# Kernel optimization log

Hardware: AMD Instinct MI355X
Metric: run time of the kernel (lower is better)

## Reference

```python
import jax, jax.numpy as jnp
import numpy as np

N, E, F_IN = 50000, 800000, 128
H, C, CLS, G = 8, 32, 16, 64
NEG_SLOPE = 0.2


def setup_inputs() -> dict:
    key = jax.random.key(0)
    ks = jax.random.split(key, 11)
    s = 0.05
    return {
        "x": jax.random.normal(ks[0], (N, F_IN), jnp.float32),
        "edge_index": jax.random.randint(ks[1], (2, E), 0, N, jnp.int32),
        "batch": jnp.sort(jax.random.randint(ks[2], (N,), 0, G, jnp.int32)),
        "W1": jax.random.normal(ks[3], (F_IN, H * C), jnp.float32) * s,
        "a1_src": jax.random.normal(ks[4], (H, C), jnp.float32) * s,
        "a1_dst": jax.random.normal(ks[5], (H, C), jnp.float32) * s,
        "b1": jax.random.normal(ks[6], (H * C,), jnp.float32) * s,
        "W2": jax.random.normal(ks[7], (H * C, CLS), jnp.float32) * s,
        "a2_src": jax.random.normal(ks[8], (1, CLS), jnp.float32) * s,
        "a2_dst": jax.random.normal(ks[9], (1, CLS), jnp.float32) * s,
        "b2": jax.random.normal(ks[10], (CLS,), jnp.float32) * s,
    }


def _gat_conv(x, src, dst, W, a_s, a_d, b, concat):
    n = x.shape[0]
    Hh, Cc = a_s.shape
    xp = (x @ W).reshape(n, Hh, Cc)                      # [N,H,C]
    al_s = jnp.einsum("nhc,hc->nh", xp, a_s)             # [N,H]
    al_d = jnp.einsum("nhc,hc->nh", xp, a_d)
    e = jax.nn.leaky_relu(al_s[src] + al_d[dst], NEG_SLOPE)  # [E,H]
    m = jax.ops.segment_max(e, dst, num_segments=n)      # segment softmax over dst
    ex = jnp.exp(e - m[dst])
    denom = jax.ops.segment_sum(ex, dst, num_segments=n)
    alpha = ex / denom[dst]                              # [E,H]
    out = jax.ops.segment_sum(xp[src] * alpha[:, :, None], dst, num_segments=n)
    out = out.reshape(n, Hh * Cc) if concat else out.mean(axis=1)
    return out + b


def reference(x, edge_index, batch, W1, a1_src, a1_dst, b1, W2, a2_src, a2_dst, b2):
    n = x.shape[0]
    loops = jnp.arange(n, dtype=edge_index.dtype)        # PyG add_self_loops=True
    ei = jnp.concatenate([edge_index, jnp.stack([loops, loops])], axis=1)
    src, dst = ei[0], ei[1]
    h = jax.nn.elu(_gat_conv(x, src, dst, W1, a1_src, a1_dst, b1, True))
    h = _gat_conv(h, src, dst, W2, a2_src, a2_dst, b2, False)
    counts = jax.ops.segment_sum(jnp.ones((n,), h.dtype), batch, num_segments=G)
    pooled = jax.ops.segment_sum(h, batch, num_segments=G) / jnp.maximum(counts, 1.0)[:, None]
    return jax.nn.log_softmax(pooled, axis=1)
```

## Files before the change

kernel.cpp:

```cpp
#include <hip/hip_runtime.h>
#include <math.h>

#define N_NODES 50000
#define N_EDGES 800000
#define FDIM 128
#define NH 8
#define NC 32
#define D1 256
#define NCLS 16
#define NGRP 64
#define NEG 0.2f
#define E_TOT (N_EDGES + N_NODES)
#define NB_N 196
#define G1_BLOCKS 782
#define E_CHUNK 4096
#define NCHUNK 196
#define NBIN 196

typedef __attribute__((ext_vector_type(8))) unsigned short u16x8;
typedef __attribute__((ext_vector_type(4))) unsigned short u16x4;
typedef __attribute__((ext_vector_type(8))) short short8;
typedef __attribute__((ext_vector_type(4))) float f32x4;

static __device__ __forceinline__ float bf2f(unsigned short u) {
    return __uint_as_float(((unsigned int)u) << 16);
}
static __device__ __forceinline__ unsigned short f2bf(float f) {
    unsigned int b = __float_as_uint(f);
    return (unsigned short)((b + 0x7FFFu + ((b >> 16) & 1u)) >> 16);
}

__global__ __launch_bounds__(256) void k_init(
    const float* __restrict__ W1, unsigned short* __restrict__ w1p,
    float* __restrict__ poolS, float* __restrict__ poolC,
    const int* __restrict__ ei, int* __restrict__ binmat) {
    __shared__ int h[NBIN];
    int c = blockIdx.x;
    for (int b = threadIdx.x; b < NBIN; b += 256) h[b] = 0;
    __syncthreads();
    int e0 = c * E_CHUNK;
    int e1 = e0 + E_CHUNK; if (e1 > N_EDGES) e1 = N_EDGES;
    for (int e = e0 + threadIdx.x; e < e1; e += 256)
        atomicAdd(&h[ei[N_EDGES + e] >> 8], 1);
    int i = blockIdx.x * 256 + threadIdx.x;
    if (i < NGRP * NCLS) poolS[i] = 0.f;
    if (i < NGRP) poolC[i] = 0.f;
    if (i < FDIM * D1) {
        int ks = i >> 13;
        int r = i & 8191;
        int nt2 = r >> 9;
        int r2 = r & 511;
        int lane = r2 >> 3, e = r2 & 7;
        int k = ks * 32 + (lane >> 4) * 8 + e;
        int col = nt2 * 16 + (lane & 15);
        w1p[i] = f2bf(W1[k * D1 + col]);
    }
    __syncthreads();
    for (int b = threadIdx.x; b < NBIN; b += 256) binmat[b * NCHUNK + c] = h[b];
}

__global__ __launch_bounds__(256) void k_binprescan(int* __restrict__ binmat,
                                                    int* __restrict__ binTot) {
    __shared__ int sh[256];
    int b = blockIdx.x, t = threadIdx.x;
    int v = (t < NCHUNK) ? binmat[b * NCHUNK + t] : 0;
    sh[t] = v;
    __syncthreads();
    for (int d = 1; d < 256; d <<= 1) {
        int tv = (t >= d) ? sh[t - d] : 0;
        __syncthreads();
        sh[t] += tv;
        __syncthreads();
    }
    if (t < NCHUNK) binmat[b * NCHUNK + t] = sh[t] - v;
    if (t == 255) binTot[b] = sh[255];
}

__global__ __launch_bounds__(256) void k_gemm1m(
    const float* __restrict__ x, const unsigned short* __restrict__ w1p,
    const float* __restrict__ a1s, const float* __restrict__ a1d,
    unsigned short* __restrict__ xp1b, float* __restrict__ al1s,
    float* __restrict__ al1d) {
    const int l = threadIdx.x & 63;
    const int wid = threadIdx.x >> 6;
    const int wr = wid >> 1, wc = wid & 1;
    const int l15 = l & 15, l4 = l >> 4;
    const int base = blockIdx.x * 64;
    const int r0 = base + wr * 32;

    f32x4 acc[2][8] = {};
#pragma unroll
    for (int ks = 0; ks < 4; ++ks) {
        const int kk = ks * 32 + l4 * 8;
        short8 af[2];
#pragma unroll
        for (int rt = 0; rt < 2; ++rt) {
            int row = r0 + rt * 16 + l15;
            float4 v0 = make_float4(0.f, 0.f, 0.f, 0.f), v1 = v0;
            if (row < N_NODES) {
                const float* xr = x + (size_t)row * FDIM + kk;
                v0 = *(const float4*)xr;
                v1 = *(const float4*)(xr + 4);
            }
            short8 a;
            a[0] = (short)f2bf(v0.x); a[1] = (short)f2bf(v0.y);
            a[2] = (short)f2bf(v0.z); a[3] = (short)f2bf(v0.w);
            a[4] = (short)f2bf(v1.x); a[5] = (short)f2bf(v1.y);
            a[6] = (short)f2bf(v1.z); a[7] = (short)f2bf(v1.w);
            af[rt] = a;
        }
#pragma unroll
        for (int nt = 0; nt < 8; ++nt) {
            int nt2 = wc * 8 + nt;
            short8 bf_ = *(const short8*)&w1p[(size_t)((ks * 16 + nt2) * 64 + l) * 8];
            acc[0][nt] = __builtin_amdgcn_mfma_f32_16x16x32_bf16(af[0], bf_, acc[0][nt], 0, 0, 0);
            acc[1][nt] = __builtin_amdgcn_mfma_f32_16x16x32_bf16(af[1], bf_, acc[1][nt], 0, 0, 0);
        }
    }
#pragma unroll
    for (int rt = 0; rt < 2; ++rt) {
        int rbase = r0 + rt * 16 + l4 * 4;
#pragma unroll
        for (int nt = 0; nt < 8; ++nt) {
            int col = wc * 128 + nt * 16 + l15;
            f32x4 c = acc[rt][nt];
#pragma unroll
            for (int r = 0; r < 4; ++r) {
                int row = rbase + r;
                if (row < N_NODES) xp1b[(size_t)row * D1 + col] = f2bf(c[r]);
            }
        }
    }
#pragma unroll
    for (int hl = 0; hl < 4; ++hl) {
        int hg = wc * 4 + hl;
        float as0 = a1s[hg * NC + l15], as1 = a1s[hg * NC + 16 + l15];
        float ad0 = a1d[hg * NC + l15], ad1 = a1d[hg * NC + 16 + l15];
#pragma unroll
        for (int rt = 0; rt < 2; ++rt) {
            f32x4 c0 = acc[rt][2 * hl], c1 = acc[rt][2 * hl + 1];
#pragma unroll
            for (int r = 0; r < 4; ++r) {
                float ss = c0[r] * as0 + c1[r] * as1;
                float dd = c0[r] * ad0 + c1[r] * ad1;
#pragma unroll
                for (int msk = 1; msk < 16; msk <<= 1) {
                    ss += __shfl_xor(ss, msk);
                    dd += __shfl_xor(dd, msk);
                }
                int row = r0 + rt * 16 + l4 * 4 + r;
                if (l15 == 0 && row < N_NODES) {
                    al1s[row * NH + hg] = ss;
                    al1d[row * NH + hg] = dd;
                }
            }
        }
    }
}

__global__ __launch_bounds__(256) void k_binscatter(const int* __restrict__ ei,
                                                    const int* __restrict__ offs,
                                                    const int* __restrict__ binTot,
                                                    int* __restrict__ binned) {
    __shared__ int cur[NBIN];
    __shared__ int sb[256];
    int c = blockIdx.x;
    int t = threadIdx.x;
    int v = (t < NBIN) ? binTot[t] : 0;
    sb[t] = v;
    __syncthreads();
    for (int d = 1; d < 256; d <<= 1) {
        int tv = (t >= d) ? sb[t - d] : 0;
        __syncthreads();
        sb[t] += tv;
        __syncthreads();
    }
    if (t < NBIN) cur[t] = (sb[t] - v) + offs[t * NCHUNK + c];
    __syncthreads();
    int e0 = c * E_CHUNK;
    int e1 = e0 + E_CHUNK; if (e1 > N_EDGES) e1 = N_EDGES;
    for (int e = e0 + t; e < e1; e += 256) {
        int s = ei[e], d = ei[N_EDGES + e];
        int pos = atomicAdd(&cur[d >> 8], 1);
        binned[pos] = s | ((d & 255) << 16);
    }
}

__global__ __launch_bounds__(256) void k_bincsr(const int* __restrict__ binTot,
                                                const int* __restrict__ binned,
                                                int* __restrict__ rowptr,
                                                int* __restrict__ cnt,
                                                int* __restrict__ esrc) {
    __shared__ int sh[256];
    __shared__ int lcnt[256];
    __shared__ int lcur[256];
    int b = blockIdx.x;
    int t = threadIdx.x;
    int v = (t < NBIN) ? binTot[t] : 0;
    sh[t] = v;
    __syncthreads();
    for (int d = 1; d < 256; d <<= 1) {
        int tv = (t >= d) ? sh[t - d] : 0;
        __syncthreads();
        sh[t] += tv;
        __syncthreads();
    }
    int estart = (b == 0) ? 0 : sh[b - 1];
    int eend = sh[b];
    __syncthreads();
    int nbase = b * 256;
    int nin = N_NODES - nbase; if (nin > 256) nin = 256;
    lcnt[t] = 0;
    __syncthreads();
    for (int e = estart + t; e < eend; e += 256)
        atomicAdd(&lcnt[(binned[e] >> 16) & 255], 1);
    __syncthreads();
    int myc = lcnt[t] + (t < nin ? 1 : 0);
    sh[t] = myc;
    __syncthreads();
    for (int d = 1; d < 256; d <<= 1) {
        int tv = (t >= d) ? sh[t - d] : 0;
        __syncthreads();
        sh[t] += tv;
        __syncthreads();
    }
    int excl = sh[t] - myc;
    int outbase = estart + nbase;
    int rp = outbase + excl;
    if (t < nin) {
        rowptr[nbase + t] = rp;
        cnt[nbase + t] = myc;
        esrc[rp] = nbase + t;
    }
    lcur[t] = rp + (t < nin ? 1 : 0);
    __syncthreads();
    for (int e = estart + t; e < eend; e += 256) {
        int vv = binned[e];
        int pos = atomicAdd(&lcur[(vv >> 16) & 255], 1);
        esrc[pos] = vv & 0xFFFF;
    }
}

__global__ __launch_bounds__(256) void k_att1(
    const unsigned short* __restrict__ xp1b, const float* __restrict__ al1s,
    const float* __restrict__ al1d, const float* __restrict__ b1,
    const int* __restrict__ rowptr, const int* __restrict__ cnt,
    const int* __restrict__ esrc, unsigned short* __restrict__ h1b) {
    __shared__ int s_src[4][64];
    __shared__ float s_alpha[4][64 * 8];
    int wv = threadIdx.x >> 6;
    int lane = threadIdx.x & 63;
    int n = blockIdx.x * 4 + wv;
    int start = rowptr[n];
    int deg = cnt[n];
    int dcap = deg < 64 ? deg : 64;
    int dpad = (dcap + 7) & ~7;
    for (int j = lane; j < dpad; j += 64)
        s_src[wv][j] = (j < dcap) ? esrc[start + j] : n;
    int npad = (dpad - dcap) * 8;
    if (lane < npad) s_alpha[wv][dcap * 8 + lane] = 0.f;
    int h = lane & 7, eg = lane >> 3;
    float ald = al1d[n * NH + h];
    float m = -1e30f;
    for (int j = eg; j < dcap; j += 8) {
        int s = s_src[wv][j];
        float v = al1s[s * NH + h] + ald;
        v = fmaxf(v, NEG * v);
        s_alpha[wv][j * 8 + h] = v;
        m = fmaxf(m, v);
    }
    if (deg > 64) {
        for (int j = 64 + eg; j < deg; j += 8) {
            int s = esrc[start + j];
            float v = al1s[s * NH + h] + ald;
            m = fmaxf(m, fmaxf(v, NEG * v));
        }
    }
    for (int msk = 8; msk < 64; msk <<= 1) m = fmaxf(m, __shfl_xor(m, msk));
    float den = 0.f;
    for (int j = eg; j < dcap; j += 8) {
        float e = __expf(s_alpha[wv][j * 8 + h] - m);
        s_alpha[wv][j * 8 + h] = e;
        den += e;
    }
    if (deg > 64) {
        for (int j = 64 + eg; j < deg; j += 8) {
            int s = esrc[start + j];
            float v = al1s[s * NH + h] + ald;
            v = fmaxf(v, NEG * v);
            den += __expf(v - m);
        }
    }
    for (int msk = 8; msk < 64; msk <<= 1) den += __shfl_xor(den, msk);
    int hh = lane >> 3;
    int cbb = lane << 3;
    float rd2 = 1.f / __shfl(den, hh);
    float m2 = __shfl(m, hh);
    float a0 = 0.f, a1 = 0.f, a2 = 0.f, a3 = 0.f;
    for (int j0 = 0; j0 < dpad; j0 += 8) {
        int off[8];
        float aw[8];
#pragma unroll
        for (int k = 0; k < 8; ++k) {
            int s = s_src[wv][j0 + k];
            aw[k] = s_alpha[wv][(j0 + k) * 8 + hh];
            off[k] = (s << 9) + cbb;
        }
#pragma unroll
        for (int k = 0; k < 8; ++k) {
            u16x4 xv = *(const u16x4*)((const char*)xp1b + off[k]);
            a0 = fmaf(aw[k], bf2f(xv[0]), a0);
            a1 = fmaf(aw[k], bf2f(xv[1]), a1);
            a2 = fmaf(aw[k], bf2f(xv[2]), a2);
            a3 = fmaf(aw[k], bf2f(xv[3]), a3);
        }
    }
    if (deg > 64) {
        float ald2 = al1d[n * NH + hh];
        for (int j = 64; j < deg; ++j) {
            int s = esrc[start + j];
            float v = al1s[s * NH + hh] + ald2;
            v = fmaxf(v, NEG * v);
            float al = __expf(v - m2);
            u16x4 xv = *(const u16x4*)((const char*)xp1b + (s << 9) + cbb);
            a0 = fmaf(al, bf2f(xv[0]), a0);
            a1 = fmaf(al, bf2f(xv[1]), a1);
            a2 = fmaf(al, bf2f(xv[2]), a2);
            a3 = fmaf(al, bf2f(xv[3]), a3);
        }
    }
    int cb = lane << 2;
    float4 bb = *(const float4*)(b1 + cb);
    a0 = fmaf(a0, rd2, bb.x);
    a1 = fmaf(a1, rd2, bb.y);
    a2 = fmaf(a2, rd2, bb.z);
    a3 = fmaf(a3, rd2, bb.w);
    a0 = a0 > 0.f ? a0 : expm1f(a0);
    a1 = a1 > 0.f ? a1 : expm1f(a1);
    a2 = a2 > 0.f ? a2 : expm1f(a2);
    a3 = a3 > 0.f ? a3 : expm1f(a3);
    u16x4 pk = { f2bf(a0), f2bf(a1), f2bf(a2), f2bf(a3) };
    *(u16x4*)(h1b + (size_t)n * D1 + cb) = pk;
}

__global__ __launch_bounds__(256) void k_gemm2(
    const unsigned short* __restrict__ h1b, const float* __restrict__ W2,
    const float* __restrict__ a2s, const float* __restrict__ a2d,
    float* __restrict__ xp2, float* __restrict__ al2s, float* __restrict__ al2d) {
    __shared__ float w2s[D1 * NCLS];
    for (int i = threadIdx.x; i < D1 * NCLS; i += 256) w2s[i] = W2[i];
    __syncthreads();
    int n = blockIdx.x * 256 + threadIdx.x;
    if (n >= N_NODES) return;
    float4 acc[4];
#pragma unroll
    for (int q = 0; q < 4; ++q) acc[q] = make_float4(0.f, 0.f, 0.f, 0.f);
    const unsigned short* hr = h1b + (size_t)n * D1;
    for (int k0 = 0; k0 < D1; k0 += 8) {
        u16x8 hv = *(const u16x8*)(hr + k0);
#pragma unroll
        for (int j = 0; j < 8; ++j) {
            float hx = bf2f(hv[j]);
#pragma unroll
            for (int q = 0; q < 4; ++q) {
                float4 w = *(const float4*)(&w2s[(k0 + j) * NCLS + q * 4]);
                acc[q].x = fmaf(hx, w.x, acc[q].x);
                acc[q].y = fmaf(hx, w.y, acc[q].y);
                acc[q].z = fmaf(hx, w.z, acc[q].z);
                acc[q].w = fmaf(hx, w.w, acc[q].w);
            }
        }
    }
    float ss = 0.f, dd = 0.f;
#pragma unroll
    for (int q = 0; q < 4; ++q) {
        *(float4*)(xp2 + (size_t)n * NCLS + q * 4) = acc[q];
        float4 s4 = *(const float4*)(a2s + q * 4);
        float4 d4 = *(const float4*)(a2d + q * 4);
        ss += acc[q].x * s4.x + acc[q].y * s4.y + acc[q].z * s4.z + acc[q].w * s4.w;
        dd += acc[q].x * d4.x + acc[q].y * d4.y + acc[q].z * d4.z + acc[q].w * d4.w;
    }
    al2s[n] = ss;
    al2d[n] = dd;
}

__global__ __launch_bounds__(256) void k_att2(
    const float* __restrict__ xp2, const float* __restrict__ al2s,
    const float* __restrict__ al2d, const float* __restrict__ b2,
    const int* __restrict__ rowptr, const int* __restrict__ cnt,
    const int* __restrict__ esrc, float* __restrict__ out2) {
    __shared__ int s_src[4][64];
    __shared__ float s_a[4][64];
    int wave = threadIdx.x >> 6;
    int lane = threadIdx.x & 63;
    int n = blockIdx.x * 4 + wave;
    int start = rowptr[n];
    int deg = cnt[n];
    int dcap = deg < 64 ? deg : 64;
    int dpad = (dcap + 7) & ~7;
    for (int j = lane; j < dpad; j += 64)
        s_src[wave][j] = (j < dcap) ? esrc[start + j] : n;
    if (lane < dpad - dcap) s_a[wave][dcap + lane] = 0.f;
    float ald = al2d[n];
    float m = -1e30f;
    for (int j = lane; j < dcap; j += 64) {
        int s = s_src[wave][j];
        float v = al2s[s] + ald;
        v = fmaxf(v, NEG * v);
        s_a[wave][j] = v;
        m = fmaxf(m, v);
    }
    if (deg > 64) {
        for (int j = 64 + lane; j < deg; j += 64) {
            float v = al2s[esrc[start + j]] + ald;
            m = fmaxf(m, fmaxf(v, NEG * v));
        }
    }
    for (int msk = 1; msk < 64; msk <<= 1) m = fmaxf(m, __shfl_xor(m, msk));
    float den = 0.f;
    for (int j = lane; j < dcap; j += 64) {
        float e = __expf(s_a[wave][j] - m);
        s_a[wave][j] = e;
        den += e;
    }
    if (deg > 64) {
        for (int j = 64 + lane; j < deg; j += 64) {
            float v = al2s[esrc[start + j]] + ald;
            v = fmaxf(v, NEG * v);
            den += __expf(v - m);
        }
    }
    for (int msk = 1; msk < 64; msk <<= 1) den += __shfl_xor(den, msk);
    float rden = 1.f / den;
    int c = lane & 15;
    int eg = lane >> 4;
    float acc = 0.f;
    for (int j0 = 0; j0 < dpad; j0 += 8) {
#pragma unroll
        for (int k = 0; k < 2; ++k) {
            int e = j0 + eg + 4 * k;
            float aw = s_a[wave][e];
            int s = s_src[wave][e];
            acc = fmaf(aw, xp2[(size_t)s * NCLS + c], acc);
        }
    }
    if (deg > 64) {
        for (int j = 64 + eg; j < deg; j += 4) {
            int s = esrc[start + j];
            float v = al2s[s] + ald;
            v = fmaxf(v, NEG * v);
            acc += __expf(v - m) * xp2[(size_t)s * NCLS + c];
        }
    }
    acc += __shfl_xor(acc, 16);
    acc += __shfl_xor(acc, 32);
    if (lane < 16) out2[(size_t)n * NCLS + lane] = acc * rden + b2[lane];
}

__global__ __launch_bounds__(256) void k_pool(
    const float* __restrict__ out2, const int* __restrict__ batch,
    float* __restrict__ poolS, float* __restrict__ poolC) {
    __shared__ float sacc[NGRP * NCLS];
    __shared__ float scnt[NGRP];
    for (int i = threadIdx.x; i < NGRP * NCLS; i += 256) sacc[i] = 0.f;
    if (threadIdx.x < NGRP) scnt[threadIdx.x] = 0.f;
    __syncthreads();
    int n = blockIdx.x * 256 + threadIdx.x;
    if (n < N_NODES) {
        int g = batch[n];
        atomicAdd(&scnt[g], 1.f);
#pragma unroll
        for (int q = 0; q < 4; ++q) {
            float4 v = *(const float4*)(out2 + (size_t)n * NCLS + q * 4);
            atomicAdd(&sacc[g * NCLS + q * 4 + 0], v.x);
            atomicAdd(&sacc[g * NCLS + q * 4 + 1], v.y);
            atomicAdd(&sacc[g * NCLS + q * 4 + 2], v.z);
            atomicAdd(&sacc[g * NCLS + q * 4 + 3], v.w);
        }
    }
    __syncthreads();
    for (int i = threadIdx.x; i < NGRP * NCLS; i += 256)
        if (sacc[i] != 0.f) atomicAdd(&poolS[i], sacc[i]);
    if (threadIdx.x < NGRP && scnt[threadIdx.x] != 0.f)
        atomicAdd(&poolC[threadIdx.x], scnt[threadIdx.x]);
}

__global__ void k_final(const float* __restrict__ poolS,
                        const float* __restrict__ poolC, float* __restrict__ out) {
    int g = threadIdx.x;
    if (g >= NGRP) return;
    float inv = 1.f / fmaxf(poolC[g], 1.f);
    float v[NCLS];
    float m = -1e30f;
#pragma unroll
    for (int c = 0; c < NCLS; ++c) {
        v[c] = poolS[g * NCLS + c] * inv;
        m = fmaxf(m, v[c]);
    }
    float s = 0.f;
#pragma unroll
    for (int c = 0; c < NCLS; ++c) s += expf(v[c] - m);
    float lse = m + logf(s);
#pragma unroll
    for (int c = 0; c < NCLS; ++c) out[g * NCLS + c] = v[c] - lse;
}

extern "C" void kernel_launch(void* const* d_in, const int* in_sizes, int n_in,
                              void* d_out, int out_size, void* d_ws, size_t ws_size,
                              hipStream_t stream) {
    const float* x    = (const float*)d_in[0];
    const int*   ei   = (const int*)d_in[1];
    const int*   batch = (const int*)d_in[2];
    const float* W1   = (const float*)d_in[3];
    const float* a1s  = (const float*)d_in[4];
    const float* a1d  = (const float*)d_in[5];
    const float* b1   = (const float*)d_in[6];
    const float* W2   = (const float*)d_in[7];
    const float* a2s  = (const float*)d_in[8];
    const float* a2d  = (const float*)d_in[9];
    const float* b2   = (const float*)d_in[10];
    float* out = (float*)d_out;

    float* f = (float*)d_ws;
    float* al1s_ = f;  f += (size_t)N_NODES * NH;
    float* al1d_ = f;  f += (size_t)N_NODES * NH;
    float* xp2   = f;  f += (size_t)N_NODES * NCLS;
    float* al2s_ = f;  f += N_NODES;
    float* al2d_ = f;  f += N_NODES;
    float* out2  = f;  f += (size_t)N_NODES * NCLS;
    float* poolS = f;  f += NGRP * NCLS;
    float* poolC = f;  f += NGRP;
    unsigned short* xp1b = (unsigned short*)f;
    unsigned short* h1b  = xp1b + (size_t)N_NODES * D1;
    unsigned short* w1p  = h1b + (size_t)N_NODES * D1;
    int* binmat  = (int*)(w1p + FDIM * D1);
    int* binTot  = binmat + NBIN * NCHUNK;
    int* binned  = binTot + NBIN;
    int* rowptr  = binned + N_EDGES;
    int* cnt     = rowptr + N_NODES;
    int* esrc    = cnt + N_NODES;

    k_init<<<NB_N, 256, 0, stream>>>(W1, w1p, poolS, poolC, ei, binmat);
    k_binprescan<<<NBIN, 256, 0, stream>>>(binmat, binTot);
    k_gemm1m<<<G1_BLOCKS, 256, 0, stream>>>(x, w1p, a1s, a1d, xp1b, al1s_, al1d_);
    k_binscatter<<<NCHUNK, 256, 0, stream>>>(ei, binmat, binTot, binned);
    k_bincsr<<<NBIN, 256, 0, stream>>>(binTot, binned, rowptr, cnt, esrc);
    k_att1<<<N_NODES / 4, 256, 0, stream>>>(xp1b, al1s_, al1d_, b1, rowptr, cnt, esrc, h1b);
    k_gemm2<<<NB_N, 256, 0, stream>>>(h1b, W2, a2s, a2d, xp2, al2s_, al2d_);
    k_att2<<<N_NODES / 4, 256, 0, stream>>>(xp2, al2s_, al2d_, b2, rowptr, cnt, esrc, out2);
    k_pool<<<NB_N, 256, 0, stream>>>(out2, batch, poolS, poolC);
    k_final<<<1, 64, 0, stream>>>(poolS, poolC, out);
}
```

Before: 192.7 us.

## Split layer-1 attention per head, fuse binscatter into GEMM1, store xp2 as bf16

Layer-1 attention now launches one block per head per four nodes. The per-head attention logits are stored head-major, so each wave handles a single head with one lane per edge. The bin-scatter kernel is folded into the GEMM1 launch as extra blocks, which removes a launch and lets it overlap with the GEMM. The layer-2 projection is stored in bf16 to halve gather traffic in att2. The per-head split trades wide vector loads for 2-byte scalar gathers and re-reads edge lists eight times, and bf16 xp2 adds rounding error.

Result: slower. 271.0 us (+40.6%).

```diff
diff --git a/kernel.cpp b/kernel.cpp
--- a/kernel.cpp
+++ b/kernel.cpp
@@ -17,8 +17,8 @@
 #define NCHUNK 196
 #define NBIN 196
 
+typedef __attribute__((ext_vector_type(4))) unsigned short u16x4;
 typedef __attribute__((ext_vector_type(8))) unsigned short u16x8;
-typedef __attribute__((ext_vector_type(4))) unsigned short u16x4;
 typedef __attribute__((ext_vector_type(8))) short short8;
 typedef __attribute__((ext_vector_type(4))) float f32x4;
 
@@ -80,7 +80,34 @@
     const float* __restrict__ x, const unsigned short* __restrict__ w1p,
     const float* __restrict__ a1s, const float* __restrict__ a1d,
     unsigned short* __restrict__ xp1b, float* __restrict__ al1s,
-    float* __restrict__ al1d) {
+    float* __restrict__ al1d, const int* __restrict__ ei,
+    const int* __restrict__ offs, const int* __restrict__ binTot,
+    int* __restrict__ binned) {
+    __shared__ int cur[NBIN];
+    __shared__ int sb[256];
+    if (blockIdx.x >= G1_BLOCKS) {
+        int c = blockIdx.x - G1_BLOCKS;
+        int t = threadIdx.x;
+        int v = (t < NBIN) ? binTot[t] : 0;
+        sb[t] = v;
+        __syncthreads();
+        for (int d = 1; d < 256; d <<= 1) {
+            int tv = (t >= d) ? sb[t - d] : 0;
+            __syncthreads();
+            sb[t] += tv;
+            __syncthreads();
+        }
+        if (t < NBIN) cur[t] = (sb[t] - v) + offs[t * NCHUNK + c];
+        __syncthreads();
+        int e0 = c * E_CHUNK;
+        int e1 = e0 + E_CHUNK; if (e1 > N_EDGES) e1 = N_EDGES;
+        for (int e = e0 + t; e < e1; e += 256) {
+            int s = ei[e], d = ei[N_EDGES + e];
+            int pos = atomicAdd(&cur[d >> 8], 1);
+            binned[pos] = s | ((d & 255) << 16);
+        }
+        return;
+    }
     const int l = threadIdx.x & 63;
     const int wid = threadIdx.x >> 6;
     const int wr = wid >> 1, wc = wid & 1;
@@ -150,39 +177,11 @@
                 }
                 int row = r0 + rt * 16 + l4 * 4 + r;
                 if (l15 == 0 && row < N_NODES) {
-                    al1s[row * NH + hg] = ss;
-                    al1d[row * NH + hg] = dd;
+                    al1s[hg * N_NODES + row] = ss;
+                    al1d[hg * N_NODES + row] = dd;
                 }
             }
         }
-    }
-}
-
-__global__ __launch_bounds__(256) void k_binscatter(const int* __restrict__ ei,
-                                                    const int* __restrict__ offs,
-                                                    const int* __restrict__ binTot,
-                                                    int* __restrict__ binned) {
-    __shared__ int cur[NBIN];
-    __shared__ int sb[256];
-    int c = blockIdx.x;
-    int t = threadIdx.x;
-    int v = (t < NBIN) ? binTot[t] : 0;
-    sb[t] = v;
-    __syncthreads();
-    for (int d = 1; d < 256; d <<= 1) {
-        int tv = (t >= d) ? sb[t - d] : 0;
-        __syncthreads();
-        sb[t] += tv;
-        __syncthreads();
-    }
-    if (t < NBIN) cur[t] = (sb[t] - v) + offs[t * NCHUNK + c];
-    __syncthreads();
-    int e0 = c * E_CHUNK;
-    int e1 = e0 + E_CHUNK; if (e1 > N_EDGES) e1 = N_EDGES;
-    for (int e = e0 + t; e < e1; e += 256) {
-        int s = ei[e], d = ei[N_EDGES + e];
-        int pos = atomicAdd(&cur[d >> 8], 1);
-        binned[pos] = s | ((d & 255) << 16);
     }
 }
 
@@ -241,112 +240,92 @@
     }
 }
 
-__global__ __launch_bounds__(256) void k_att1(
+__global__ __launch_bounds__(256) void k_att1s(
     const unsigned short* __restrict__ xp1b, const float* __restrict__ al1s,
     const float* __restrict__ al1d, const float* __restrict__ b1,
     const int* __restrict__ rowptr, const int* __restrict__ cnt,
     const int* __restrict__ esrc, unsigned short* __restrict__ h1b) {
     __shared__ int s_src[4][64];
-    __shared__ float s_alpha[4][64 * 8];
+    __shared__ float s_alpha[4][64];
     int wv = threadIdx.x >> 6;
     int lane = threadIdx.x & 63;
-    int n = blockIdx.x * 4 + wv;
+    int hh = blockIdx.x & 7;
+    int n = (blockIdx.x >> 3) * 4 + wv;
     int start = rowptr[n];
     int deg = cnt[n];
     int dcap = deg < 64 ? deg : 64;
     int dpad = (dcap + 7) & ~7;
-    for (int j = lane; j < dpad; j += 64)
-        s_src[wv][j] = (j < dcap) ? esrc[start + j] : n;
-    int npad = (dpad - dcap) * 8;
-    if (lane < npad) s_alpha[wv][dcap * 8 + lane] = 0.f;
-    int h = lane & 7, eg = lane >> 3;
-    float ald = al1d[n * NH + h];
-    float m = -1e30f;
-    for (int j = eg; j < dcap; j += 8) {
-        int s = s_src[wv][j];
-        float v = al1s[s * NH + h] + ald;
-        v = fmaxf(v, NEG * v);
-        s_alpha[wv][j * 8 + h] = v;
-        m = fmaxf(m, v);
-    }
+    const float* alsc = al1s + (size_t)hh * N_NODES;
+    float ald = al1d[(size_t)hh * N_NODES + n];
+    int s0 = n;
+    float v = -1e30f;
+    if (lane < dcap) {
+        s0 = esrc[start + lane];
+        float t = alsc[s0] + ald;
+        v = fmaxf(t, NEG * t);
+    }
+    s_src[wv][lane] = (lane < dcap) ? s0 : n;
+    float m = v;
     if (deg > 64) {
-        for (int j = 64 + eg; j < deg; j += 8) {
+        for (int j = 64 + lane; j < deg; j += 64) {
+            float t = alsc[esrc[start + j]] + ald;
+            m = fmaxf(m, fmaxf(t, NEG * t));
+        }
+    }
+    for (int msk = 1; msk < 64; msk <<= 1) m = fmaxf(m, __shfl_xor(m, msk));
+    float a = (lane < dcap) ? __expf(v - m) : 0.f;
+    s_alpha[wv][lane] = a;
+    float den = a;
+    if (deg > 64) {
+        for (int j = 64 + lane; j < deg; j += 64) {
+            float t = alsc[esrc[start + j]] + ald;
+            t = fmaxf(t, NEG * t);
+            den += __expf(t - m);
+        }
+    }
+    for (int msk = 1; msk < 64; msk <<= 1) den += __shfl_xor(den, msk);
+    float rd = 1.f / den;
+    int e2 = lane >> 5, c = lane & 31;
+    const int cbb = (hh * 32 + c) * 2;
+    float acc = 0.f;
+    for (int j0 = 0; j0 < dpad; j0 += 8) {
+        float aw[4]; int off[4];
+#pragma unroll
+        for (int k = 0; k < 4; ++k) {
+            int e = j0 + e2 + 2 * k;
+            int s = s_src[wv][e];
+            aw[k] = s_alpha[wv][e];
+            off[k] = (s << 9) + cbb;
+        }
+#pragma unroll
+        for (int k = 0; k < 4; ++k) {
+            unsigned short xv = *(const unsigned short*)((const char*)xp1b + off[k]);
+            acc = fmaf(aw[k], bf2f(xv), acc);
+        }
+    }
+    if (deg > 64) {
+        for (int j = 64 + e2; j < deg; j += 2) {
             int s = esrc[start + j];
-            float v = al1s[s * NH + h] + ald;
-            m = fmaxf(m, fmaxf(v, NEG * v));
-        }
-    }
-    for (int msk = 8; msk < 64; msk <<= 1) m = fmaxf(m, __shfl_xor(m, msk));
-    float den = 0.f;
-    for (int j = eg; j < dcap; j += 8) {
-        float e = __expf(s_alpha[wv][j * 8 + h] - m);
-        s_alpha[wv][j * 8 + h] = e;
-        den += e;
-    }
-    if (deg > 64) {
-        for (int j = 64 + eg; j < deg; j += 8) {
-            int s = esrc[start + j];
-            float v = al1s[s * NH + h] + ald;
-            v = fmaxf(v, NEG * v);
-            den += __expf(v - m);
-        }
-    }
-    for (int msk = 8; msk < 64; msk <<= 1) den += __shfl_xor(den, msk);
-    int hh = lane >> 3;
-    int cbb = lane << 3;
-    float rd2 = 1.f / __shfl(den, hh);
-    float m2 = __shfl(m, hh);
-    float a0 = 0.f, a1 = 0.f, a2 = 0.f, a3 = 0.f;
-    for (int j0 = 0; j0 < dpad; j0 += 8) {
-        int off[8];
-        float aw[8];
-#pragma unroll
-        for (int k = 0; k < 8; ++k) {
-            int s = s_src[wv][j0 + k];
-            aw[k] = s_alpha[wv][(j0 + k) * 8 + hh];
-            off[k] = (s << 9) + cbb;
-        }
-#pragma unroll
-        for (int k = 0; k < 8; ++k) {
-            u16x4 xv = *(const u16x4*)((const char*)xp1b + off[k]);
-            a0 = fmaf(aw[k], bf2f(xv[0]), a0);
-            a1 = fmaf(aw[k], bf2f(xv[1]), a1);
-            a2 = fmaf(aw[k], bf2f(xv[2]), a2);
-            a3 = fmaf(aw[k], bf2f(xv[3]), a3);
-        }
-    }
-    if (deg > 64) {
-        float ald2 = al1d[n * NH + hh];
-        for (int j = 64; j < deg; ++j) {
-            int s = esrc[start + j];
-            float v = al1s[s * NH + hh] + ald2;
-            v = fmaxf(v, NEG * v);
-            float al = __expf(v - m2);
-            u16x4 xv = *(const u16x4*)((const char*)xp1b + (s << 9) + cbb);
-            a0 = fmaf(al, bf2f(xv[0]), a0);
-            a1 = fmaf(al, bf2f(xv[1]), a1);
-            a2 = fmaf(al, bf2f(xv[2]), a2);
-            a3 = fmaf(al, bf2f(xv[3]), a3);
-        }
-    }
-    int cb = lane << 2;
-    float4 bb = *(const float4*)(b1 + cb);
-    a0 = fmaf(a0, rd2, bb.x);
-    a1 = fmaf(a1, rd2, bb.y);
-    a2 = fmaf(a2, rd2, bb.z);
-    a3 = fmaf(a3, rd2, bb.w);
-    a0 = a0 > 0.f ? a0 : expm1f(a0);
-    a1 = a1 > 0.f ? a1 : expm1f(a1);
-    a2 = a2 > 0.f ? a2 : expm1f(a2);
-    a3 = a3 > 0.f ? a3 : expm1f(a3);
-    u16x4 pk = { f2bf(a0), f2bf(a1), f2bf(a2), f2bf(a3) };
-    *(u16x4*)(h1b + (size_t)n * D1 + cb) = pk;
+            float t = alsc[s] + ald;
+            t = fmaxf(t, NEG * t);
+            float al = __expf(t - m);
+            unsigned short xv = *(const unsigned short*)((const char*)xp1b + (s << 9) + cbb);
+            acc = fmaf(al, bf2f(xv), acc);
+        }
+    }
+    acc += __shfl_xor(acc, 32);
+    if (e2 == 0) {
+        float hv = fmaf(acc, rd, b1[hh * NC + c]);
+        hv = hv > 0.f ? hv : expm1f(hv);
+        h1b[(size_t)n * D1 + hh * NC + c] = f2bf(hv);
+    }
 }
 
 __global__ __launch_bounds__(256) void k_gemm2(
     const unsigned short* __restrict__ h1b, const float* __restrict__ W2,
     const float* __restrict__ a2s, const float* __restrict__ a2d,
-    float* __restrict__ xp2, float* __restrict__ al2s, float* __restrict__ al2d) {
+    unsigned short* __restrict__ xp2b, float* __restrict__ al2s,
+    float* __restrict__ al2d) {
     __shared__ float w2s[D1 * NCLS];
     for (int i = threadIdx.x; i < D1 * NCLS; i += 256) w2s[i] = W2[i];
     __syncthreads();
@@ -372,20 +351,30 @@
         }
     }
     float ss = 0.f, dd = 0.f;
+    u16x8 pk0, pk1;
 #pragma unroll
     for (int q = 0; q < 4; ++q) {
-        *(float4*)(xp2 + (size_t)n * NCLS + q * 4) = acc[q];
         float4 s4 = *(const float4*)(a2s + q * 4);
         float4 d4 = *(const float4*)(a2d + q * 4);
         ss += acc[q].x * s4.x + acc[q].y * s4.y + acc[q].z * s4.z + acc[q].w * s4.w;
         dd += acc[q].x * d4.x + acc[q].y * d4.y + acc[q].z * d4.z + acc[q].w * d4.w;
     }
+    pk0[0] = f2bf(acc[0].x); pk0[1] = f2bf(acc[0].y);
+    pk0[2] = f2bf(acc[0].z); pk0[3] = f2bf(acc[0].w);
+    pk0[4] = f2bf(acc[1].x); pk0[5] = f2bf(acc[1].y);
+    pk0[6] = f2bf(acc[1].z); pk0[7] = f2bf(acc[1].w);
+    pk1[0] = f2bf(acc[2].x); pk1[1] = f2bf(acc[2].y);
+    pk1[2] = f2bf(acc[2].z); pk1[3] = f2bf(acc[2].w);
+    pk1[4] = f2bf(acc[3].x); pk1[5] = f2bf(acc[3].y);
+    pk1[6] = f2bf(acc[3].z); pk1[7] = f2bf(acc[3].w);
+    *(u16x8*)(xp2b + (size_t)n * NCLS) = pk0;
+    *(u16x8*)(xp2b + (size_t)n * NCLS + 8) = pk1;
     al2s[n] = ss;
     al2d[n] = dd;
 }
 
 __global__ __launch_bounds__(256) void k_att2(
-    const float* __restrict__ xp2, const float* __restrict__ al2s,
+    const unsigned short* __restrict__ xp2b, const float* __restrict__ al2s,
     const float* __restrict__ al2d, const float* __restrict__ b2,
     const int* __restrict__ rowptr, const int* __restrict__ cnt,
     const int* __restrict__ esrc, float* __restrict__ out2) {
@@ -441,7 +430,7 @@
             int e = j0 + eg + 4 * k;
             float aw = s_a[wave][e];
             int s = s_src[wave][e];
-            acc = fmaf(aw, xp2[(size_t)s * NCLS + c], acc);
+            acc = fmaf(aw, bf2f(xp2b[(size_t)s * NCLS + c]), acc);
         }
     }
     if (deg > 64) {
@@ -449,7 +438,7 @@
             int s = esrc[start + j];
             float v = al2s[s] + ald;
             v = fmaxf(v, NEG * v);
-            acc += __expf(v - m) * xp2[(size_t)s * NCLS + c];
+            acc += __expf(v - m) * bf2f(xp2b[(size_t)s * NCLS + c]);
         }
     }
     acc += __shfl_xor(acc, 16);
@@ -524,7 +513,6 @@
     float* f = (float*)d_ws;
     float* al1s_ = f;  f += (size_t)N_NODES * NH;
     float* al1d_ = f;  f += (size_t)N_NODES * NH;
-    float* xp2   = f;  f += (size_t)N_NODES * NCLS;
     float* al2s_ = f;  f += N_NODES;
     float* al2d_ = f;  f += N_NODES;
     float* out2  = f;  f += (size_t)N_NODES * NCLS;
@@ -532,7 +520,8 @@
     float* poolC = f;  f += NGRP;
     unsigned short* xp1b = (unsigned short*)f;
     unsigned short* h1b  = xp1b + (size_t)N_NODES * D1;
-    unsigned short* w1p  = h1b + (size_t)N_NODES * D1;
+    unsigned short* xp2b = h1b + (size_t)N_NODES * D1;
+    unsigned short* w1p  = xp2b + (size_t)N_NODES * NCLS;
     int* binmat  = (int*)(w1p + FDIM * D1);
     int* binTot  = binmat + NBIN * NCHUNK;
     int* binned  = binTot + NBIN;
@@ -542,12 +531,14 @@
 
     k_init<<<NB_N, 256, 0, stream>>>(W1, w1p, poolS, poolC, ei, binmat);
     k_binprescan<<<NBIN, 256, 0, stream>>>(binmat, binTot);
-    k_gemm1m<<<G1_BLOCKS, 256, 0, stream>>>(x, w1p, a1s, a1d, xp1b, al1s_, al1d_);
-    k_binscatter<<<NCHUNK, 256, 0, stream>>>(ei, binmat, binTot, binned);
+    k_gemm1m<<<G1_BLOCKS + NCHUNK, 256, 0, stream>>>(x, w1p, a1s, a1d, xp1b,
+                                                     al1s_, al1d_, ei, binmat,
+                                                     binTot, binned);
     k_bincsr<<<NBIN, 256, 0, stream>>>(binTot, binned, rowptr, cnt, esrc);
-    k_att1<<<N_NODES / 4, 256, 0, stream>>>(xp1b, al1s_, al1d_, b1, rowptr, cnt, esrc, h1b);
-    k_gemm2<<<NB_N, 256, 0, stream>>>(h1b, W2, a2s, a2d, xp2, al2s_, al2d_);
-    k_att2<<<N_NODES / 4, 256, 0, stream>>>(xp2, al2s_, al2d_, b2, rowptr, cnt, esrc, out2);
+    k_att1s<<<(N_NODES / 4) * 8, 256, 0, stream>>>(xp1b, al1s_, al1d_, b1,
+                                                   rowptr, cnt, esrc, h1b);
+    k_gemm2<<<NB_N, 256, 0, stream>>>(h1b, W2, a2s, a2d, xp2b, al2s_, al2d_);
+    k_att2<<<N_NODES / 4, 256, 0, stream>>>(xp2b, al2s_, al2d_, b2, rowptr, cnt, esrc, out2);
     k_pool<<<NB_N, 256, 0, stream>>>(out2, batch, poolS, poolC);
     k_final<<<1, 64, 0, stream>>>(poolS, poolC, out);
 }
```
